# Performance work log

Measured on AMD Instinct MI355X. Metric: run time of the kernel, lower is better.

Reference implementation:

```python
import jax, jax.numpy as jnp
import numpy as np

NUM_HEADS = 16


def setup_inputs() -> dict:
    key = jax.random.key(0)
    ks = jax.random.split(key, 5)
    B, S, E = 4, 2048, 1024
    scale = 1.0 / np.sqrt(E)
    return {
        "query": jax.random.normal(ks[0], (B, S, E), dtype=jnp.float32),
        "w_in": jax.random.normal(ks[1], (3 * E, E), dtype=jnp.float32) * scale,
        "b_in": jax.random.normal(ks[2], (3 * E,), dtype=jnp.float32) * 0.02,
        "w_out": jax.random.normal(ks[3], (E, E), dtype=jnp.float32) * scale,
        "b_out": jax.random.normal(ks[4], (E,), dtype=jnp.float32) * 0.02,
    }


def reference(query, w_in, b_in, w_out, b_out):
    B, S, E = query.shape
    H = NUM_HEADS
    D = E // H
    # fused QKV projection: [B,S,3E]
    qkv = jnp.einsum('bse,fe->bsf', query, w_in) + b_in
    q, k, v = jnp.split(qkv, 3, axis=-1)
    # [B,H,S,D]
    q = q.reshape(B, S, H, D).transpose(0, 2, 1, 3)
    k = k.reshape(B, S, H, D).transpose(0, 2, 1, 3)
    v = v.reshape(B, S, H, D).transpose(0, 2, 1, 3)
    # scaled dot-product attention with causal mask (is_causal=True, dropout=0)
    scores = jnp.einsum('bhqd,bhkd->bhqk', q, k) * (1.0 / np.sqrt(D))
    causal = jnp.tril(jnp.ones((S, S), dtype=bool))
    scores = jnp.where(causal, scores, jnp.finfo(scores.dtype).min)
    probs = jax.nn.softmax(scores, axis=-1)
    attn = jnp.einsum('bhqk,bhkd->bhqd', probs, v)
    attn = attn.transpose(0, 2, 1, 3).reshape(B, S, E)
    return jnp.einsum('bse,fe->bsf', attn, w_out) + b_out
```

## Files before the change

kernel.cpp:

```cpp
#include <hip/hip_runtime.h>

typedef __bf16 bf16;
typedef __bf16 bf16x4 __attribute__((ext_vector_type(4)));
typedef __bf16 bf16x8 __attribute__((ext_vector_type(8)));
typedef float  f32x4  __attribute__((ext_vector_type(4)));
typedef short  short4v __attribute__((ext_vector_type(4)));

#define GLOAD_LDS16(g, l) __builtin_amdgcn_global_load_lds( \
    (const __attribute__((address_space(1))) void*)(g),     \
    (__attribute__((address_space(3))) void*)(l), 16, 0, 0)

__device__ __forceinline__ float exp2_hw(float x) { return __builtin_amdgcn_exp2f(x); }

#if __has_builtin(__builtin_amdgcn_mfma_f32_16x16x16bf16_1k)
__device__ __forceinline__ f32x4 mfma16(bf16x4 a, bf16x4 b, f32x4 c) {
    return __builtin_amdgcn_mfma_f32_16x16x16bf16_1k(
        __builtin_bit_cast(short4v, a), __builtin_bit_cast(short4v, b), c, 0, 0, 0);
}
#elif __has_builtin(__builtin_amdgcn_mfma_f32_16x16x16_bf16)
__device__ __forceinline__ f32x4 mfma16(bf16x4 a, bf16x4 b, f32x4 c) {
    return __builtin_amdgcn_mfma_f32_16x16x16_bf16(a, b, c, 0, 0, 0);
}
#else
__device__ __forceinline__ f32x4 mfma16(bf16x4 a, bf16x4 b, f32x4 c) {
    asm volatile("v_mfma_f32_16x16x16_bf16 %0, %1, %2, %0"
                 : "+v"(c) : "v"(a), "v"(b));
    return c;
}
#endif

__global__ __launch_bounds__(256) void f32_to_bf16(
    const float* __restrict__ in, bf16* __restrict__ out, int n4)
{
    int i = blockIdx.x * blockDim.x + threadIdx.x;
    const int stride = gridDim.x * blockDim.x;
    for (; i < n4; i += stride) {
        const float4 v = *(const float4*)(in + (size_t)i * 4);
        bf16x4 o = { (bf16)v.x, (bf16)v.y, (bf16)v.z, (bf16)v.w };
        *(bf16x4*)(out + (size_t)i * 4) = o;
    }
}

__global__ __launch_bounds__(256) void conv_rest(
    const float* __restrict__ w_in_f, const float* __restrict__ b_in_f,
    const float* __restrict__ w_out_f, const float* __restrict__ b_out_f,
    bf16* __restrict__ w_in, bf16* __restrict__ b_in,
    bf16* __restrict__ w_out, bf16* __restrict__ b_out)
{
    constexpr int N1 = 786432, N2 = N1 + 768, N3 = N2 + 262144, N4 = N3 + 256;
    int i = blockIdx.x * blockDim.x + threadIdx.x;
    const int stride = gridDim.x * blockDim.x;
    for (; i < N4; i += stride) {
        const float* src; bf16* dst; int off;
        if (i < N1)      { src = w_in_f;  dst = w_in;  off = i; }
        else if (i < N2) { src = b_in_f;  dst = b_in;  off = i - N1; }
        else if (i < N3) { src = w_out_f; dst = w_out; off = i - N2; }
        else             { src = b_out_f; dst = b_out; off = i - N3; }
        const float4 v = *(const float4*)(src + (size_t)off * 4);
        bf16x4 o = { (bf16)v.x, (bf16)v.y, (bf16)v.z, (bf16)v.w };
        *(bf16x4*)(dst + (size_t)off * 4) = o;
    }
}

__device__ __forceinline__ void gemm_mainloop_128(
    const bf16* __restrict__ A, const bf16* __restrict__ B, int K,
    int bm, int bn, bf16* As, bf16* Bs, f32x4 (&acc)[4][4])
{
    const int tid  = threadIdx.x;
    const int lane = tid & 63, fr = lane & 15, fq = lane >> 4;
    const int wave = tid >> 6;
    const int wr   = (wave >> 1) * 64, wc = (wave & 1) * 64;
    const int srow = tid >> 3, sj = tid & 7;
    const int sjs  = (sj ^ (srow & 7)) * 8;
    const int xo0  = (fq ^ (fr & 7)) * 8;
    const int xo1  = ((4 + fq) ^ (fr & 7)) * 8;

    const bf16* Ag = A + (size_t)(bm * 128 + srow) * K + sjs;
    const bf16* Bg = B + (size_t)(bn * 128 + srow) * K + sjs;
    bf16* Asw = As + srow * 64 + sj * 8;
    bf16* Bsw = Bs + srow * 64 + sj * 8;

    for (int k0 = 0; k0 < K; k0 += 64) {
        __syncthreads();
#pragma unroll
        for (int it = 0; it < 4; ++it)
            GLOAD_LDS16(Ag + k0 + (size_t)it * 32 * K, Asw + it * 32 * 64);
#pragma unroll
        for (int it = 0; it < 4; ++it)
            GLOAD_LDS16(Bg + k0 + (size_t)it * 32 * K, Bsw + it * 32 * 64);
        asm volatile("s_waitcnt vmcnt(0)" ::: "memory");
        __syncthreads();

#pragma unroll
        for (int ks = 0; ks < 2; ++ks) {
            const int xo = ks ? xo1 : xo0;
            bf16x8 a[4], b[4];
#pragma unroll
            for (int m = 0; m < 4; ++m)
                a[m] = *(const bf16x8*)&As[(wr + m * 16 + fr) * 64 + xo];
#pragma unroll
            for (int n = 0; n < 4; ++n)
                b[n] = *(const bf16x8*)&Bs[(wc + n * 16 + fr) * 64 + xo];
#pragma unroll
            for (int m = 0; m < 4; ++m)
#pragma unroll
                for (int n = 0; n < 4; ++n)
                    acc[m][n] = __builtin_amdgcn_mfma_f32_16x16x32_bf16(a[m], b[n], acc[m][n], 0, 0, 0);
        }
    }
}

__global__ __launch_bounds__(256) void gemm_qkv(
    const bf16* __restrict__ A, const bf16* __restrict__ B,
    const bf16* __restrict__ bias,
    bf16* __restrict__ qb_, bf16* __restrict__ kb_, bf16* __restrict__ vt_)
{
    constexpr int K = 1024, NTN = 24;
    constexpr float QSCALE = 0.18033688011112042f;
    __shared__ bf16 As[128 * 64];
    __shared__ bf16 Bs[128 * 64];
    const int bm = blockIdx.x / NTN, bn = blockIdx.x % NTN;

    f32x4 acc[4][4] = {};
    gemm_mainloop_128(A, B, K, bm, bn, As, Bs, acc);

    const int tid = threadIdx.x, lane = tid & 63;
    const int fr = lane & 15, fq = lane >> 4;
    const int wave = tid >> 6;
    const int wr = (wave >> 1) * 64, wc = (wave & 1) * 64;

    const int colbase = bn * 128 + wc;
    const int part = colbase >> 10;

#pragma unroll
    for (int n = 0; n < 4; ++n) {
        const int col = colbase + n * 16 + fr;
        const float bv = (float)bias[col];
        const int cl = col & 1023, h = cl >> 6, d = cl & 63;
#pragma unroll
        for (int m = 0; m < 4; ++m) {
            const int row0 = bm * 128 + wr + m * 16 + fq * 4;
            const int bb = row0 >> 11, s0 = row0 & 2047;
            const int bh = bb * 16 + h;
            if (part == 0) {
#pragma unroll
                for (int j = 0; j < 4; ++j)
                    qb_[((size_t)bh * 2048 + s0 + j) * 64 + d] = (bf16)((acc[m][n][j] + bv) * QSCALE);
            } else if (part == 1) {
#pragma unroll
                for (int j = 0; j < 4; ++j)
                    kb_[((size_t)bh * 2048 + s0 + j) * 64 + d] = (bf16)(acc[m][n][j] + bv);
            } else {
                bf16x4 o;
#pragma unroll
                for (int j = 0; j < 4; ++j) o[j] = (bf16)(acc[m][n][j] + bv);
                *(bf16x4*)&vt_[((size_t)bh * 64 + d) * 2048 + s0] = o;
            }
        }
    }
}

__global__ __launch_bounds__(256) void gemm_out(
    const bf16* __restrict__ A, const bf16* __restrict__ B,
    const bf16* __restrict__ bias, float* __restrict__ C)
{
    constexpr int K = 1024, N = 1024, NTN = 8;
    __shared__ bf16 As[128 * 64];
    __shared__ bf16 Bs[128 * 64];
    const int bm = blockIdx.x / NTN, bn = blockIdx.x % NTN;

    f32x4 acc[4][4] = {};
    gemm_mainloop_128(A, B, K, bm, bn, As, Bs, acc);

    const int tid = threadIdx.x, lane = tid & 63;
    const int fr = lane & 15, fq = lane >> 4;
    const int wave = tid >> 6;
    const int wr = (wave >> 1) * 64, wc = (wave & 1) * 64;

#pragma unroll
    for (int n = 0; n < 4; ++n) {
        const int col = bn * 128 + wc + n * 16 + fr;
        const float bv = (float)bias[col];
#pragma unroll
        for (int m = 0; m < 4; ++m) {
            const int row0 = bm * 128 + wr + m * 16 + fq * 4;
#pragma unroll
            for (int j = 0; j < 4; ++j)
                C[(size_t)(row0 + j) * N + col] = acc[m][n][j] + bv;
        }
    }
}

__global__ __launch_bounds__(512, 4) void attn8(
    const bf16* __restrict__ qb_, const bf16* __restrict__ kb_,
    const bf16* __restrict__ vt_, bf16* __restrict__ ctx)
{
    constexpr int S = 2048, EO = 1024;
    constexpr float NEG = -3.0e38f;
    __shared__ bf16 Ks[2][64 * 64];
    __shared__ bf16 Vs[2][64 * 64];

    const int idx = blockIdx.x;
    const int orig = (idx & 7) * 64 + (idx >> 3);
    const int bh = orig >> 3;
    const int p  = orig & 7;
    const int bb = bh >> 4, h = bh & 15;

    const int tid = threadIdx.x, lane = tid & 63, wave = tid >> 6;
    const int fr = lane & 15, fq = lane >> 4;

    const bf16* kh = kb_ + (size_t)bh * S * 64;
    const bf16* vh = vt_ + (size_t)bh * 64 * S;
    const bf16* qh = qb_ + (size_t)bh * S * 64;

    const int xo0 = (fq ^ (fr & 7)) * 8;
    const int xo1 = ((4 + fq) ^ (fr & 7)) * 8;

    int krb[4], vslot[4], vrow[4];
#pragma unroll
    for (int n = 0; n < 4; ++n) {
        krb[n]   = (n * 16 + fr) * 64;
        vslot[n] = ((n * 2 + (fq >> 1)) ^ (fr & 7)) * 8 + (fq & 1) * 4;
        vrow[n]  = (n * 16 + fr) * 64;
    }

    const int r0 = tid >> 3, j0 = tid & 7;
    const int js = (j0 ^ (r0 & 7)) * 8;

#define STAGE(buf, kt)                                                        \
    do {                                                                      \
        GLOAD_LDS16(kh + (size_t)((kt) * 64 + r0) * 64 + js,                  \
                    &Ks[buf][(r0 * 8 + j0) * 8]);                             \
        GLOAD_LDS16(vh + (size_t)r0 * S + (kt) * 64 + js,                     \
                    &Vs[buf][(r0 * 8 + j0) * 8]);                             \
    } while (0)

    const bf16 one = (bf16)1.0f;
    const bf16x4 ones = { one, one, one, one };

#pragma unroll
    for (int sub = 0; sub < 2; ++sub) {
        const int qb = sub ? p : (15 - p);
        const int q0 = qb * 128 + wave * 16;

        bf16x8 qf0, qf1;
        {
            const bf16* qr = qh + (size_t)(q0 + fr) * 64;
            qf0 = *(const bf16x8*)(qr + fq * 8);
            qf1 = *(const bf16x8*)(qr + 32 + fq * 8);
        }

        f32x4 acc[4] = {};
        f32x4 acc1 = {};

        const int ktend = 2 * qb + 1;

        STAGE(0, 0);
        asm volatile("s_waitcnt vmcnt(0)" ::: "memory");
        __syncthreads();

        int cur = 0;
        for (int kt = 0; kt <= ktend; ++kt) {
            if (kt < ktend) STAGE(cur ^ 1, kt + 1);

            const int nmax = (q0 + 15 - kt * 64) >> 4;
            if (nmax >= 0) {
                f32x4 s[4];
                __builtin_amdgcn_s_setprio(1);
#pragma unroll
                for (int n = 0; n < 4; ++n) {
                    if (n > nmax) continue;
                    s[n] = f32x4{};
                    bf16x8 k0v = *(const bf16x8*)&Ks[cur][krb[n] + xo0];
                    bf16x8 k1v = *(const bf16x8*)&Ks[cur][krb[n] + xo1];
                    s[n] = __builtin_amdgcn_mfma_f32_16x16x32_bf16(k0v, qf0, s[n], 0, 0, 0);
                    s[n] = __builtin_amdgcn_mfma_f32_16x16x32_bf16(k1v, qf1, s[n], 0, 0, 0);
                }
                __builtin_amdgcn_s_setprio(0);

                if (nmax <= 3) {
                    const int qrel = q0 - kt * 64 + fr;
#pragma unroll
                    for (int n = 0; n < 4; ++n) {
                        if (n > nmax) continue;
#pragma unroll
                        for (int j = 0; j < 4; ++j)
                            if (n * 16 + fq * 4 + j > qrel) s[n][j] = NEG;
                    }
                }

                bf16x4 pb[4];
#pragma unroll
                for (int n = 0; n < 4; ++n) {
                    if (n > nmax) continue;
                    pb[n][0] = (bf16)exp2_hw(s[n][0]);
                    pb[n][1] = (bf16)exp2_hw(s[n][1]);
                    pb[n][2] = (bf16)exp2_hw(s[n][2]);
                    pb[n][3] = (bf16)exp2_hw(s[n][3]);
                    acc1 = mfma16(pb[n], ones, acc1);
                }

                __builtin_amdgcn_s_setprio(1);
#pragma unroll
                for (int n = 0; n < 4; ++n) {
                    if (n > nmax) continue;
#pragma unroll
                    for (int n2 = 0; n2 < 4; ++n2) {
                        bf16x4 vf = *(const bf16x4*)&Vs[cur][vrow[n2] + vslot[n]];
                        acc[n2] = mfma16(pb[n], vf, acc[n2]);
                    }
                }
                __builtin_amdgcn_s_setprio(0);
            }

            asm volatile("s_waitcnt vmcnt(0)" ::: "memory");
            __syncthreads();
            cur ^= 1;
        }

        float linv[4];
#pragma unroll
        for (int j = 0; j < 4; ++j) linv[j] = __builtin_amdgcn_rcpf(acc1[j]);

#pragma unroll
        for (int n2 = 0; n2 < 4; ++n2)
#pragma unroll
            for (int j = 0; j < 4; ++j) {
                int qr_ = q0 + fq * 4 + j;
                ctx[((size_t)bb * S + qr_) * EO + h * 64 + n2 * 16 + fr] =
                    (bf16)(acc[n2][j] * linv[j]);
            }
    }
#undef STAGE
}

extern "C" void kernel_launch(void* const* d_in, const int* in_sizes, int n_in,
                              void* d_out, int out_size, void* d_ws, size_t ws_size,
                              hipStream_t stream)
{
    constexpr int B = 4, S = 2048, E = 1024;
    constexpr int M = B * S;
    constexpr size_t N_Q  = (size_t)B * S * E;
    constexpr size_t N_WI = (size_t)3 * E * E;
    constexpr size_t N_BI = 3 * E;
    constexpr size_t N_WO = (size_t)E * E;

    const float* query_f = (const float*)d_in[0];
    const float* w_in_f  = (const float*)d_in[1];
    const float* b_in_f  = (const float*)d_in[2];
    const float* w_out_f = (const float*)d_in[3];
    const float* b_out_f = (const float*)d_in[4];
    float* out = (float*)d_out;

    bf16* q_buf = (bf16*)d_ws;
    bf16* k_buf = q_buf + N_Q;
    bf16* vT    = k_buf + N_Q;
    bf16* ctx   = vT + N_Q;
    bf16* query = ctx + N_Q;
    bf16* w_in  = query + N_Q;
    bf16* b_in  = w_in + N_WI;
    bf16* w_out = b_in + N_BI;
    bf16* b_out = w_out + N_WO;

    f32_to_bf16<<<2048, 256, 0, stream>>>(query_f, query, (int)(N_Q / 4));
    conv_rest<<<1024, 256, 0, stream>>>(w_in_f, b_in_f, w_out_f, b_out_f,
                                        w_in, b_in, w_out, b_out);

    gemm_qkv<<<dim3((M / 128) * (3 * E / 128)), 256, 0, stream>>>(
        query, w_in, b_in, q_buf, k_buf, vT);

    attn8<<<dim3(512), 512, 0, stream>>>(q_buf, k_buf, vT, ctx);

    gemm_out<<<dim3((M / 128) * (E / 128)), 256, 0, stream>>>(
        ctx, w_out, b_out, out);
}
```

Before: 165.1 us.

## Triple-buffer attention K/V staging and merge conversion kernels into one launch

The attention kernel moves from double to triple buffering of the K and V tiles in shared memory. It prefetches two tiles ahead and waits with a partial vmcnt, so each iteration needs only one barrier instead of a full drain at the end. The two fp32-to-bf16 conversion kernels are merged into a single launch, removing one kernel launch. The cost is more LDS per block (48KB instead of 32KB), which could limit occupancy at 4 blocks per CU, and the vmcnt(2) count must match the number of loads issued per STAGE.

```diff
diff --git a/kernel.cpp b/kernel.cpp
--- a/kernel.cpp
+++ b/kernel.cpp
@@ -29,33 +29,27 @@
 }
 #endif
 
-__global__ __launch_bounds__(256) void f32_to_bf16(
-    const float* __restrict__ in, bf16* __restrict__ out, int n4)
-{
-    int i = blockIdx.x * blockDim.x + threadIdx.x;
-    const int stride = gridDim.x * blockDim.x;
-    for (; i < n4; i += stride) {
-        const float4 v = *(const float4*)(in + (size_t)i * 4);
-        bf16x4 o = { (bf16)v.x, (bf16)v.y, (bf16)v.z, (bf16)v.w };
-        *(bf16x4*)(out + (size_t)i * 4) = o;
-    }
-}
-
-__global__ __launch_bounds__(256) void conv_rest(
-    const float* __restrict__ w_in_f, const float* __restrict__ b_in_f,
-    const float* __restrict__ w_out_f, const float* __restrict__ b_out_f,
-    bf16* __restrict__ w_in, bf16* __restrict__ b_in,
-    bf16* __restrict__ w_out, bf16* __restrict__ b_out)
-{
-    constexpr int N1 = 786432, N2 = N1 + 768, N3 = N2 + 262144, N4 = N3 + 256;
+__global__ __launch_bounds__(256) void conv_all(
+    const float* __restrict__ q_f, const float* __restrict__ wi_f,
+    const float* __restrict__ bi_f, const float* __restrict__ wo_f,
+    const float* __restrict__ bo_f,
+    bf16* __restrict__ q_o, bf16* __restrict__ wi_o, bf16* __restrict__ bi_o,
+    bf16* __restrict__ wo_o, bf16* __restrict__ bo_o)
+{
+    constexpr int N0 = 2097152;
+    constexpr int N1 = N0 + 786432;
+    constexpr int N2 = N1 + 768;
+    constexpr int N3 = N2 + 262144;
+    constexpr int N4 = N3 + 256;
     int i = blockIdx.x * blockDim.x + threadIdx.x;
     const int stride = gridDim.x * blockDim.x;
     for (; i < N4; i += stride) {
         const float* src; bf16* dst; int off;
-        if (i < N1)      { src = w_in_f;  dst = w_in;  off = i; }
-        else if (i < N2) { src = b_in_f;  dst = b_in;  off = i - N1; }
-        else if (i < N3) { src = w_out_f; dst = w_out; off = i - N2; }
-        else             { src = b_out_f; dst = b_out; off = i - N3; }
+        if (i < N0)      { src = q_f;  dst = q_o;  off = i; }
+        else if (i < N1) { src = wi_f; dst = wi_o; off = i - N0; }
+        else if (i < N2) { src = bi_f; dst = bi_o; off = i - N1; }
+        else if (i < N3) { src = wo_f; dst = wo_o; off = i - N2; }
+        else             { src = bo_f; dst = bo_o; off = i - N3; }
         const float4 v = *(const float4*)(src + (size_t)off * 4);
         bf16x4 o = { (bf16)v.x, (bf16)v.y, (bf16)v.z, (bf16)v.w };
         *(bf16x4*)(dst + (size_t)off * 4) = o;
@@ -191,14 +185,14 @@
     }
 }
 
-__global__ __launch_bounds__(512, 4) void attn8(
+__global__ __launch_bounds__(512, 4) void attn9(
     const bf16* __restrict__ qb_, const bf16* __restrict__ kb_,
     const bf16* __restrict__ vt_, bf16* __restrict__ ctx)
 {
     constexpr int S = 2048, EO = 1024;
     constexpr float NEG = -3.0e38f;
-    __shared__ bf16 Ks[2][64 * 64];
-    __shared__ bf16 Vs[2][64 * 64];
+    __shared__ bf16 Ks[3][64 * 64];
+    __shared__ bf16 Vs[3][64 * 64];
 
     const int idx = blockIdx.x;
     const int orig = (idx & 7) * 64 + (idx >> 3);
@@ -255,13 +249,19 @@
 
         const int ktend = 2 * qb + 1;
 
+        __syncthreads();
         STAGE(0, 0);
-        asm volatile("s_waitcnt vmcnt(0)" ::: "memory");
-        __syncthreads();
+        STAGE(1, 1);
 
         int cur = 0;
         for (int kt = 0; kt <= ktend; ++kt) {
-            if (kt < ktend) STAGE(cur ^ 1, kt + 1);
+            if (kt < ktend)
+                asm volatile("s_waitcnt vmcnt(2)" ::: "memory");
+            else
+                asm volatile("s_waitcnt vmcnt(0)" ::: "memory");
+            __syncthreads();
+
+            if (kt + 2 <= ktend) STAGE((kt + 2) % 3, kt + 2);
 
             const int nmax = (q0 + 15 - kt * 64) >> 4;
             if (nmax >= 0) {
@@ -313,9 +313,7 @@
                 __builtin_amdgcn_s_setprio(0);
             }
 
-            asm volatile("s_waitcnt vmcnt(0)" ::: "memory");
-            __syncthreads();
-            cur ^= 1;
+            cur = (cur + 1) % 3;
         }
 
         float linv[4];
@@ -362,14 +360,13 @@
     bf16* w_out = b_in + N_BI;
     bf16* b_out = w_out + N_WO;
 
-    f32_to_bf16<<<2048, 256, 0, stream>>>(query_f, query, (int)(N_Q / 4));
-    conv_rest<<<1024, 256, 0, stream>>>(w_in_f, b_in_f, w_out_f, b_out_f,
-                                        w_in, b_in, w_out, b_out);
+    conv_all<<<2048, 256, 0, stream>>>(query_f, w_in_f, b_in_f, w_out_f, b_out_f,
+                                       query, w_in, b_in, w_out, b_out);
 
     gemm_qkv<<<dim3((M / 128) * (3 * E / 128)), 256, 0, stream>>>(
         query, w_in, b_in, q_buf, k_buf, vT);
 
-    attn8<<<dim3(512), 512, 0, stream>>>(q_buf, k_buf, vT, ctx);
+    attn9<<<dim3(512), 512, 0, stream>>>(q_buf, k_buf, vT, ctx);
 
     gemm_out<<<dim3((M / 128) * (E / 128)), 256, 0, stream>>>(
         ctx, w_out, b_out, out);
```

New measurement: 164.6 us. No clear change (-0.3%).
